# Performance work log

Hardware: AMD Instinct MI355X
Metric: run time of the kernel (lower is better)

## Reference

```python
import jax, jax.numpy as jnp
import numpy as np

N = 100000   # nodes
E = 300000   # edges
D = 256      # emb_dim
FD = 512     # feat_dim
L = 5        # num_layer
G = 4000     # num graphs
NUM_ATOM = 100
NUM_BOND = 2
EPS = 1e-5


def setup_inputs() -> dict:
    key = jax.random.key(0)
    ks = jax.random.split(key, 24)
    s = 0.02
    inp = {
        "atomics": jax.random.randint(ks[0], (N,), 0, NUM_ATOM, dtype=jnp.int32),
        "pos": jax.random.normal(ks[1], (N, 3), dtype=jnp.float32),
        "edge_index": jax.random.randint(ks[2], (2, E), 0, N, dtype=jnp.int32),
        "edge_attr": jax.random.randint(ks[3], (E,), 0, NUM_BOND, dtype=jnp.int32),
        "batch": jnp.sort(jax.random.randint(ks[4], (N,), 0, G, dtype=jnp.int32)),
        # parameters
        "x_emb1": jax.random.normal(ks[5], (NUM_ATOM, D)) * s,
        "x_emb2_w": jax.random.normal(ks[6], (3, D)) * s,
        "x_emb2_b": jnp.zeros((D,), jnp.float32),
        "edge_emb": jax.random.normal(ks[7], (L, NUM_BOND, D)) * s,
        "mlp_w1": jax.random.normal(ks[8], (L, D, 2 * D)) * s,
        "mlp_b1": jnp.zeros((L, 2 * D), jnp.float32),
        "mlp_w2": jax.random.normal(ks[9], (L, 2 * D, D)) * s,
        "mlp_b2": jnp.zeros((L, D), jnp.float32),
        "bn_gamma": jnp.ones((L, D), jnp.float32),
        "bn_beta": jnp.zeros((L, D), jnp.float32),
        "feat_w": jax.random.normal(ks[10], (D, FD)) * s,
        "feat_b": jnp.zeros((FD,), jnp.float32),
        "head_w1": jax.random.normal(ks[11], (FD, FD // 2)) * s,
        "head_b1": jnp.zeros((FD // 2,), jnp.float32),
        "head_w2": jax.random.normal(ks[12], (FD // 2, 1)) * s,
        "head_b2": jnp.zeros((1,), jnp.float32),
    }
    return inp


def reference(atomics, pos, edge_index, edge_attr, batch,
              x_emb1, x_emb2_w, x_emb2_b, edge_emb,
              mlp_w1, mlp_b1, mlp_w2, mlp_b2, bn_gamma, bn_beta,
              feat_w, feat_b, head_w1, head_b1, head_w2, head_b2):
    n = atomics.shape[0]
    # initial node features: atom-type embedding + linear(pos)
    h = x_emb1[atomics] + pos @ x_emb2_w + x_emb2_b
    # add self loops (self-loop bond type = NUM_BOND-1)
    loop = jnp.arange(n, dtype=edge_index.dtype)
    src = jnp.concatenate([edge_index[0], loop])           # x_j (source)
    dst = jnp.concatenate([edge_index[1], loop])           # aggregate target
    eattr = jnp.concatenate([edge_attr,
                             jnp.full((n,), NUM_BOND - 1, dtype=edge_attr.dtype)])
    for l in range(L):
        msg = h[src] + edge_emb[l][eattr]                  # [E+N, D]
        agg = jax.ops.segment_sum(msg, dst, num_segments=n)
        # GINEConv MLP: Linear -> Softplus -> Linear
        h = jax.nn.softplus(agg @ mlp_w1[l] + mlp_b1[l]) @ mlp_w2[l] + mlp_b2[l]
        # BatchNorm1d (training mode: batch statistics, biased var)
        mean = h.mean(axis=0)
        var = h.var(axis=0)
        h = (h - mean) / jnp.sqrt(var + EPS) * bn_gamma[l] + bn_beta[l]
        if l < L - 1:
            h = jax.nn.softplus(h)
        # dropout with drop_ratio=0 is a no-op
    feat = h @ feat_w + feat_b                             # [N, FD]
    # global mean pool over graphs
    ssum = jax.ops.segment_sum(feat, batch, num_segments=G)
    cnt = jax.ops.segment_sum(jnp.ones((n,), feat.dtype), batch, num_segments=G)
    gfeat = ssum / jnp.maximum(cnt, 1.0)[:, None]          # [G, FD]
    hid = jax.nn.softplus(gfeat @ head_w1 + head_b1)
    return hid @ head_w2 + head_b2                          # [G, 1]
```

## Files before the change

kernel.cpp:

```cpp
#include <hip/hip_runtime.h>
#include <hip/hip_bf16.h>
#include <hip/hip_fp16.h>
#include <stdint.h>

#define D_  256
#define FD_ 512
#define L_  5
#define EPS_ 1e-5f

#define PLANE_SH 1056
#define TILE_SH  4224

typedef unsigned short ushort_t;
typedef __attribute__((ext_vector_type(8))) _Float16 h8v;
typedef __attribute__((ext_vector_type(4))) float    f4v;

__device__ __forceinline__ float sp(float x) {
    float t = __expf(-fabsf(x));
    return fmaxf(x, 0.f) + __logf(1.f + t);
}

__device__ __forceinline__ ushort_t f2h_bits(float v) {
    union { _Float16 h; ushort_t u; } c;
    c.h = (_Float16)v;
    return c.u;
}

__device__ __forceinline__ float h2f(ushort_t u) {
    union { ushort_t u; _Float16 h; } c;
    c.u = u;
    return (float)c.h;
}

__device__ __forceinline__ size_t pk_off(int gm, int gn, int nKB) {
    return ((size_t)(gm >> 7) * nKB + (gn >> 5)) * TILE_SH
         + (size_t)((gn >> 3) & 3) * PLANE_SH
         + (gm & 127) * 8 + (gn & 7);
}

__global__ __launch_bounds__(256)
void init_h_kernel(const int* __restrict__ atomics, const float* __restrict__ pos,
                   const float* __restrict__ emb1, const float* __restrict__ w2,
                   const float* __restrict__ b2, ushort_t* __restrict__ h16, int N)
{
    int i = blockIdx.x;
    int d = threadIdx.x;
    int a = atomics[i];
    float p0 = pos[(size_t)i * 3 + 0];
    float p1 = pos[(size_t)i * 3 + 1];
    float p2 = pos[(size_t)i * 3 + 2];
    float v = emb1[(size_t)a * D_ + d]
            + p0 * w2[0 * D_ + d]
            + p1 * w2[1 * D_ + d]
            + p2 * w2[2 * D_ + d]
            + b2[d];
    h16[(size_t)i * D_ + d] = f2h_bits(v);
}

__global__ __launch_bounds__(256)
void hist_kernel(const int* __restrict__ dst, int* __restrict__ cnt, int E)
{
    int e = blockIdx.x * 256 + threadIdx.x;
    if (e < E) atomicAdd(&cnt[dst[e]], 1);
}

__global__ __launch_bounds__(256)
void alloc_kernel(const int* __restrict__ cnt, int* __restrict__ start,
                  int* __restrict__ cursor, int* __restrict__ total, int N)
{
    int i = blockIdx.x * 256 + threadIdx.x;
    if (i < N) {
        int s = atomicAdd(total, cnt[i]);
        start[i] = s;
        cursor[i] = s;
    }
}

__global__ __launch_bounds__(256)
void fill_kernel(const int* __restrict__ src, const int* __restrict__ dst,
                 const int* __restrict__ attr, int* __restrict__ cursor,
                 uint32_t* __restrict__ elist, int E)
{
    int e = blockIdx.x * 256 + threadIdx.x;
    if (e < E) {
        int p = atomicAdd(&cursor[dst[e]], 1);
        elist[p] = (uint32_t)src[e] | ((uint32_t)attr[e] << 30);
    }
}

__global__ __launch_bounds__(256)
void range_kernel(const int* __restrict__ batch, int* __restrict__ gstart,
                  int* __restrict__ gend, int N)
{
    int i = blockIdx.x * 256 + threadIdx.x;
    if (i >= N) return;
    int b = batch[i];
    if (i == 0 || batch[i - 1] != b) gstart[b] = i;
    if (i == N - 1 || batch[i + 1] != b) gend[b] = i + 1;
}

__global__ __launch_bounds__(256)
void act16_kernel(const ushort_t* __restrict__ h16, ushort_t* __restrict__ hact,
                  const float* __restrict__ bnsum, const float* __restrict__ gamma,
                  const float* __restrict__ beta, long long total8, float invN)
{
    __shared__ float ssc[256], ssh[256];
    int t = threadIdx.x;
    {
        float mean = bnsum[t] * invN;
        float var = bnsum[D_ + t] * invN - mean * mean;
        float sc = gamma[t] * rsqrtf(fmaxf(var, 0.f) + EPS_);
        ssc[t] = sc;
        ssh[t] = beta[t] - mean * sc;
    }
    __syncthreads();
    long long idx = (long long)blockIdx.x * 256 + t;
    if (idx >= total8) return;
    int c0 = (int)((idx * 8) & 255);
    uint4 in = *(const uint4*)(h16 + idx * 8);
    ushort_t* ip = (ushort_t*)&in;
    ushort_t ov[8];
#pragma unroll
    for (int j = 0; j < 8; ++j)
        ov[j] = f2h_bits(sp(h2f(ip[j]) * ssc[c0 + j] + ssh[c0 + j]));
    *(uint4*)(hact + idx * 8) = *(uint4*)ov;
}

__global__ __launch_bounds__(256)
void gather_pack4_kernel(const ushort_t* __restrict__ hact, const uint32_t* __restrict__ elist,
                         const int* __restrict__ start, const int* __restrict__ cnt,
                         const float* __restrict__ ee_l, ushort_t* __restrict__ aggP, int N)
{
    int i0 = blockIdx.x * 4;
    int d = threadIdx.x;
    float ee0 = ee_l[d];
    float ee1 = ee_l[D_ + d];
    float acc[4];
#pragma unroll
    for (int r = 0; r < 4; ++r) {
        int i = i0 + r;
        if (i >= N) { acc[r] = 0.f; continue; }
        float a = h2f(hact[(size_t)i * D_ + d]) + ee1;
        int base = start[i], deg = cnt[i];
        for (int j = 0; j < deg; ++j) {
            uint32_t p = elist[base + j];
            int s = p & 0x3FFFFFFF;
            a += h2f(hact[(size_t)s * D_ + d]) + ((p >> 30) ? ee1 : ee0);
        }
        acc[r] = a;
    }
#pragma unroll
    for (int r = 0; r < 4; ++r) {
        int i = i0 + r;
        if (i < N) aggP[pk_off(i, d, 8)] = f2h_bits(acc[r]);
    }
}

__global__ __launch_bounds__(256)
void pool_bn_kernel(const ushort_t* __restrict__ h16, const float* __restrict__ bnsum,
                    const float* __restrict__ gamma, const float* __restrict__ beta,
                    const int* __restrict__ gstart, const int* __restrict__ gend,
                    ushort_t* __restrict__ poolP, float invN)
{
    int g = blockIdx.x;
    int d = threadIdx.x;
    float mean = bnsum[d] * invN;
    float var = bnsum[D_ + d] * invN - mean * mean;
    float sc = gamma[d] * rsqrtf(fmaxf(var, 0.f) + EPS_);
    float sh = beta[d] - mean * sc;
    int s0 = gstart[g], s1 = gend[g];
    float acc = 0.f;
    int i = s0;
    for (; i + 4 <= s1; i += 4) {
        float a0 = h2f(h16[(size_t)(i + 0) * D_ + d]);
        float a1 = h2f(h16[(size_t)(i + 1) * D_ + d]);
        float a2 = h2f(h16[(size_t)(i + 2) * D_ + d]);
        float a3 = h2f(h16[(size_t)(i + 3) * D_ + d]);
        acc += (a0 + a1) + (a2 + a3);
    }
    for (; i < s1; ++i)
        acc += h2f(h16[(size_t)i * D_ + d]);
    int cnt = s1 - s0;
    float mval = (cnt > 0) ? (sc * acc / (float)cnt + sh) : 0.f;
    poolP[pk_off(g, d, 8)] = f2h_bits(mval);
}

__global__ __launch_bounds__(256)
void convert_w_pack(const float* __restrict__ W, ushort_t* __restrict__ dh,
                    int N, int nKB)
{
    int kb = blockIdx.x, nb = blockIdx.y;
    int n = threadIdx.x >> 1, half = threadIdx.x & 1;
#pragma unroll
    for (int j = 0; j < 2; ++j) {
        int kq = half * 2 + j;
        size_t o = (size_t)(nb * nKB + kb) * TILE_SH + kq * PLANE_SH + n * 8;
#pragma unroll
        for (int jj = 0; jj < 8; ++jj) {
            float w = W[(size_t)(kb * 32 + kq * 8 + jj) * N + nb * 128 + n];
            dh[o + jj] = f2h_bits(w);
        }
    }
}

__global__ __launch_bounds__(512, 4)
void fused_mlp_kernel(const ushort_t* __restrict__ APK,
                      const ushort_t* __restrict__ W1P,
                      const ushort_t* __restrict__ W2P,
                      const float* __restrict__ b1,
                      const float* __restrict__ b2,
                      ushort_t* __restrict__ Hout,
                      float* __restrict__ bnsum,
                      int m)
{
    __shared__ ushort_t Tl[32768];

    int rb = blockIdx.x;
    int tid = threadIdx.x, w = tid >> 6, lane = tid & 63;
    int fr = lane & 15, kq = lane >> 4;

    const ushort_t* aT = APK + (size_t)(rb >> 1) * (8 * TILE_SH)
                       + (size_t)kq * PLANE_SH + (size_t)((rb & 1) * 64 + fr) * 8;
    const ushort_t* bT = W1P + (size_t)(w >> 1) * (8 * TILE_SH)
                       + (size_t)kq * PLANE_SH + (size_t)((w & 1) * 64 + fr) * 8;

    f4v acc1[4][4];
#pragma unroll
    for (int i = 0; i < 4; ++i)
#pragma unroll
        for (int j = 0; j < 4; ++j)
            acc1[i][j] = (f4v){0.f, 0.f, 0.f, 0.f};

    for (int kb = 0; kb < 8; ++kb) {
        h8v Af[4], Bf[4];
#pragma unroll
        for (int t = 0; t < 4; ++t) {
            Af[t] = *(const h8v*)(aT + (size_t)kb * TILE_SH + t * 128);
            Bf[t] = *(const h8v*)(bT + (size_t)kb * TILE_SH + t * 128);
        }
        __builtin_amdgcn_s_setprio(1);
#pragma unroll
        for (int rt = 0; rt < 4; ++rt)
#pragma unroll
            for (int ct = 0; ct < 4; ++ct)
                acc1[rt][ct] = __builtin_amdgcn_mfma_f32_16x16x32_f16(
                    Af[rt], Bf[ct], acc1[rt][ct], 0, 0, 0);
        __builtin_amdgcn_s_setprio(0);
    }

#pragma unroll
    for (int ct = 0; ct < 4; ++ct) {
        float bv = b1[w * 64 + ct * 16 + fr];
        int base = (w * 2 + (ct >> 1)) * 2048
                 + ((( fr >> 3) + ct * 2) & 3) * 512
                 + (fr & 7);
#pragma unroll
        for (int rt = 0; rt < 4; ++rt)
#pragma unroll
            for (int rr = 0; rr < 4; ++rr) {
                int row = rt * 16 + kq * 4 + rr;
                Tl[base + row * 8] = f2h_bits(sp(acc1[rt][ct][rr] + bv));
            }
    }
    __syncthreads();

    const ushort_t* wT = W2P + (size_t)(w >> 2) * (16 * TILE_SH)
                       + (size_t)kq * PLANE_SH + (size_t)((w & 3) * 32 + fr) * 8;

    f4v acc2[4][2];
#pragma unroll
    for (int i = 0; i < 4; ++i)
#pragma unroll
        for (int j = 0; j < 2; ++j)
            acc2[i][j] = (f4v){0.f, 0.f, 0.f, 0.f};

    for (int kb = 0; kb < 16; ++kb) {
        h8v Tf[4], Wf[2];
#pragma unroll
        for (int t = 0; t < 4; ++t)
            Tf[t] = *(const h8v*)(Tl + kb * 2048 + kq * 512 + (fr + t * 16) * 8);
#pragma unroll
        for (int t = 0; t < 2; ++t)
            Wf[t] = *(const h8v*)(wT + (size_t)kb * TILE_SH + t * 128);
        __builtin_amdgcn_s_setprio(1);
#pragma unroll
        for (int rt = 0; rt < 4; ++rt)
#pragma unroll
            for (int ct = 0; ct < 2; ++ct)
                acc2[rt][ct] = __builtin_amdgcn_mfma_f32_16x16x32_f16(
                    Tf[rt], Wf[ct], acc2[rt][ct], 0, 0, 0);
        __builtin_amdgcn_s_setprio(0);
    }

    int gm0 = rb * 64 + kq * 4;
#pragma unroll
    for (int ct = 0; ct < 2; ++ct) {
        int gn = w * 32 + ct * 16 + fr;
        float bv = b2[gn];
        float s = 0.f, ss = 0.f;
#pragma unroll
        for (int rt = 0; rt < 4; ++rt)
#pragma unroll
            for (int rr = 0; rr < 4; ++rr) {
                int gm = gm0 + rt * 16 + rr;
                if (gm < m) {
                    float v = acc2[rt][ct][rr] + bv;
                    Hout[(size_t)gm * D_ + gn] = f2h_bits(v);
                    s += v;
                    ss += v * v;
                }
            }
        s  += __shfl_xor(s, 16);  s  += __shfl_xor(s, 32);
        ss += __shfl_xor(ss, 16); ss += __shfl_xor(ss, 32);
        if (kq == 0) {
            atomicAdd(&bnsum[gn], s);
            atomicAdd(&bnsum[D_ + gn], ss);
        }
    }
}

template <int EPI>
__global__ __launch_bounds__(256, 3)
void gemm_p16(const ushort_t* __restrict__ APK, const ushort_t* __restrict__ BPK,
              const float* __restrict__ bias,
              ushort_t* __restrict__ Tout, float* __restrict__ Cout,
              float* __restrict__ bnsum, const int* __restrict__ batch,
              int m, int N, int nKB)
{
    const int NB = N >> 7;
    const int mb = (m + 127) >> 7;
    int id = blockIdx.x;
    int grp = id / (8 * NB);
    int rem = id - grp * 8 * NB;
    int nb = rem >> 3;
    int rb = grp * 8 + (rem & 7);
    if (rb >= mb) return;

    int tid = threadIdx.x, wave = tid >> 6, lane = tid & 63;
    int wr = wave >> 1, wc = wave & 1;
    int fr = lane & 15, kq = lane >> 4;

    const ushort_t* aP = APK + (size_t)rb * nKB * TILE_SH
                       + (size_t)kq * PLANE_SH + (size_t)(wr * 64 + fr) * 8;
    const ushort_t* bP = BPK + (size_t)nb * nKB * TILE_SH
                       + (size_t)kq * PLANE_SH + (size_t)(wc * 64 + fr) * 8;

    f4v acc[4][4];
#pragma unroll
    for (int i = 0; i < 4; ++i)
#pragma unroll
        for (int j = 0; j < 4; ++j)
            acc[i][j] = (f4v){0.f, 0.f, 0.f, 0.f};

    h8v Fa[4], Fb[4], Ga[4], Gb[4];

#define LOADF(dA, dB, kbi)                                                   \
    {   const ushort_t* ap_ = aP + (size_t)(kbi) * TILE_SH;                  \
        const ushort_t* bp_ = bP + (size_t)(kbi) * TILE_SH;                  \
        _Pragma("unroll")                                                    \
        for (int t = 0; t < 4; ++t) {                                        \
            dA[t] = *(const h8v*)(ap_ + t * 128);                            \
            dB[t] = *(const h8v*)(bp_ + t * 128);                            \
        } }

#define MFMA16(sA, sB)                                                       \
    {   __builtin_amdgcn_s_setprio(1);                                       \
        _Pragma("unroll")                                                    \
        for (int rt = 0; rt < 4; ++rt)                                       \
            _Pragma("unroll")                                                \
            for (int ct = 0; ct < 4; ++ct)                                   \
                acc[rt][ct] = __builtin_amdgcn_mfma_f32_16x16x32_f16(        \
                    sA[rt], sB[ct], acc[rt][ct], 0, 0, 0);                   \
        __builtin_amdgcn_s_setprio(0); }

    LOADF(Fa, Fb, 0);
    for (int kb = 0; kb < nKB; kb += 2) {
        LOADF(Ga, Gb, kb + 1);
        MFMA16(Fa, Fb);
        if (kb + 2 < nKB) LOADF(Fa, Fb, kb + 2);
        MFMA16(Ga, Gb);
    }
#undef LOADF
#undef MFMA16

    int gm00 = rb * 128 + wr * 64 + kq * 4;
    int gn0  = nb * 128 + wc * 64 + fr;
    int nKBo = N >> 5;
    size_t tileRow = (size_t)(rb * nKBo + nb * 4 + wc * 2) * TILE_SH
                   + (size_t)((wr * 64 + kq * 4) * 8 + (fr & 7));
#pragma unroll
    for (int ct = 0; ct < 4; ++ct) {
        int gn = gn0 + ct * 16;
        float bv = bias[gn];
        float s = 0.f, ss = 0.f;
        size_t cb = tileRow + (size_t)(ct >> 1) * TILE_SH
                  + (size_t)((2 * ct + (fr >> 3)) & 3) * PLANE_SH;
#pragma unroll
        for (int rt = 0; rt < 4; ++rt) {
            if (EPI == 2) {
                int bp = -1; float run = 0.f;
#pragma unroll
                for (int rr = 0; rr < 4; ++rr) {
                    int gm = gm00 + rt * 16 + rr;
                    if (gm >= m) continue;
                    float v = acc[rt][ct][rr] + bv;
                    int bg = batch[gm];
                    if (bg == bp) { run += v; }
                    else {
                        if (bp >= 0) atomicAdd(&Cout[(size_t)bp * N + gn], run);
                        bp = bg; run = v;
                    }
                }
                if (bp >= 0) atomicAdd(&Cout[(size_t)bp * N + gn], run);
            } else {
#pragma unroll
                for (int rr = 0; rr < 4; ++rr) {
                    int gm = gm00 + rt * 16 + rr;
                    if (gm >= m) continue;
                    float v = acc[rt][ct][rr] + bv;
                    if (EPI == 0) {
                        Tout[cb + (rt * 16 + rr) * 8] = f2h_bits(sp(v));
                    } else if (EPI == 1) {
                        Tout[(size_t)gm * N + gn] = f2h_bits(v);
                        s += v;
                        ss += v * v;
                    } else {
                        Cout[(size_t)gm * N + gn] = v;
                    }
                }
            }
        }
        if (EPI == 1) {
            s  += __shfl_xor(s, 16);  s  += __shfl_xor(s, 32);
            ss += __shfl_xor(ss, 16); ss += __shfl_xor(ss, 32);
            if (kq == 0) {
                atomicAdd(&bnsum[gn], s);
                atomicAdd(&bnsum[D_ + gn], ss);
            }
        }
    }
}

#define BM 64
#define BN 64
#define BK 16

__global__ __launch_bounds__(256)
void gemm_head(const float* __restrict__ A, const float* __restrict__ W,
               const float* __restrict__ bias, float* __restrict__ C,
               int M, int N, int K)
{
    __shared__ float As[BK][BM + 4];
    __shared__ float Ws[BK][BN + 4];

    int tid = threadIdx.x;
    int bm = blockIdx.y * BM;
    int bn = blockIdx.x * BN;
    int tx = tid & 15;
    int ty = tid >> 4;

    float acc[4][4] = {};

    int a_m = tid >> 2;
    int a_k = (tid & 3) * 4;
    int w_k = tid >> 4;
    int w_n = (tid & 15) * 4;

    for (int k0 = 0; k0 < K; k0 += BK) {
        int gm = bm + a_m;
        float4 av = make_float4(0.f, 0.f, 0.f, 0.f);
        if (gm < M)
            av = *(const float4*)(A + (size_t)gm * K + k0 + a_k);
        As[a_k + 0][a_m] = av.x;
        As[a_k + 1][a_m] = av.y;
        As[a_k + 2][a_m] = av.z;
        As[a_k + 3][a_m] = av.w;

        float4 wv = *(const float4*)(W + (size_t)(k0 + w_k) * N + bn + w_n);
        *(float4*)&Ws[w_k][w_n] = wv;

        __syncthreads();

#pragma unroll
        for (int k = 0; k < BK; ++k) {
            float4 a4 = *(const float4*)&As[k][ty * 4];
            float4 b4 = *(const float4*)&Ws[k][tx * 4];
            float a[4] = {a4.x, a4.y, a4.z, a4.w};
            float b[4] = {b4.x, b4.y, b4.z, b4.w};
#pragma unroll
            for (int i = 0; i < 4; ++i)
#pragma unroll
                for (int j = 0; j < 4; ++j)
                    acc[i][j] += a[i] * b[j];
        }
        __syncthreads();
    }

#pragma unroll
    for (int i = 0; i < 4; ++i) {
        int gm = bm + ty * 4 + i;
        if (gm >= M) continue;
#pragma unroll
        for (int j = 0; j < 4; ++j) {
            int gn = bn + tx * 4 + j;
            C[(size_t)gm * N + gn] = sp(acc[i][j] + bias[gn]);
        }
    }
}

__global__ __launch_bounds__(256)
void head2_kernel(const float* __restrict__ hid, const float* __restrict__ w2,
                  const float* __restrict__ b2, float* __restrict__ out, int G)
{
    __shared__ float red[256];
    int g = blockIdx.x;
    int t = threadIdx.x;
    float v = hid[(size_t)g * 256 + t] * w2[t];
    red[t] = v;
    __syncthreads();
    for (int s = 128; s > 0; s >>= 1) {
        if (t < s) red[t] += red[t + s];
        __syncthreads();
    }
    if (t == 0) out[g] = red[0] + b2[0];
}

extern "C" void kernel_launch(void* const* d_in, const int* in_sizes, int n_in,
                              void* d_out, int out_size, void* d_ws, size_t ws_size,
                              hipStream_t stream)
{
    const int N = in_sizes[0];
    const int E = in_sizes[3];
    const int G = out_size;

    const int*   atomics  = (const int*)d_in[0];
    const float* pos      = (const float*)d_in[1];
    const int*   eidx     = (const int*)d_in[2];
    const int*   eattr    = (const int*)d_in[3];
    const int*   batch    = (const int*)d_in[4];
    const float* x_emb1   = (const float*)d_in[5];
    const float* x_emb2_w = (const float*)d_in[6];
    const float* x_emb2_b = (const float*)d_in[7];
    const float* edge_emb = (const float*)d_in[8];
    const float* mlp_w1   = (const float*)d_in[9];
    const float* mlp_b1   = (const float*)d_in[10];
    const float* mlp_w2   = (const float*)d_in[11];
    const float* mlp_b2   = (const float*)d_in[12];
    const float* bn_g     = (const float*)d_in[13];
    const float* bn_b     = (const float*)d_in[14];
    const float* feat_w   = (const float*)d_in[15];
    const float* feat_b   = (const float*)d_in[16];
    const float* head_w1  = (const float*)d_in[17];
    const float* head_b1  = (const float*)d_in[18];
    const float* head_w2  = (const float*)d_in[19];
    const float* head_b2  = (const float*)d_in[20];
    float* out = (float*)d_out;

    const int* src = eidx;
    const int* dst = eidx + E;

    char* ws = (char*)d_ws;
    size_t off = 0;
    auto carve = [&](size_t bytes) {
        void* p = ws + off;
        off += (bytes + 255) & ~(size_t)255;
        return p;
    };

    const int nRB = (N + 127) / 128;
    const int nGB = (G + 127) / 128;

    ushort_t* h16  = (ushort_t*)carve((size_t)N * D_ * 2);
    ushort_t* hact = (ushort_t*)carve((size_t)N * D_ * 2);
    ushort_t* aggP = (ushort_t*)carve((size_t)nRB * 8 * TILE_SH * 2);
    const size_t WTILES = 32 * TILE_SH;
    ushort_t* w1P = (ushort_t*)carve((size_t)L_ * WTILES * 2);
    ushort_t* w2P = (ushort_t*)carve((size_t)L_ * WTILES * 2);
    ushort_t* fP  = (ushort_t*)carve(WTILES * 2);
    float* bnsum  = (float*)carve(2 * D_ * 4);
    float* gfeat  = (float*)carve((size_t)G * FD_ * 4);
    float* hid    = (float*)carve((size_t)G * (FD_ / 2) * 4);
    ushort_t* poolP = (ushort_t*)carve((size_t)nGB * 8 * TILE_SH * 2);
    int* gstart  = (int*)carve((size_t)G * 4);
    int* gend    = (int*)carve((size_t)G * 4);
    int* cnt_i   = (int*)carve((size_t)N * 4);
    int* start_i = (int*)carve((size_t)N * 4);
    int* cursor  = (int*)carve((size_t)N * 4);
    int* total   = (int*)carve(4);
    uint32_t* elist = (uint32_t*)carve((size_t)E * 4);

    const float invN = 1.f / (float)N;

    hipMemsetAsync(cnt_i, 0, (size_t)N * 4, stream);
    hipMemsetAsync(total, 0, 4, stream);
    hipMemsetAsync(gstart, 0, (size_t)G * 4, stream);
    hipMemsetAsync(gend, 0, (size_t)G * 4, stream);
    hist_kernel<<<(E + 255) / 256, 256, 0, stream>>>(dst, cnt_i, E);
    alloc_kernel<<<(N + 255) / 256, 256, 0, stream>>>(cnt_i, start_i, cursor, total, N);
    fill_kernel<<<(E + 255) / 256, 256, 0, stream>>>(src, dst, eattr, cursor, elist, E);
    range_kernel<<<(N + 255) / 256, 256, 0, stream>>>(batch, gstart, gend, N);

    for (int l = 0; l < L_; ++l) {
        convert_w_pack<<<dim3(8, 4), 256, 0, stream>>>(
            mlp_w1 + (size_t)l * D_ * FD_, w1P + (size_t)l * WTILES, FD_, 8);
        convert_w_pack<<<dim3(16, 2), 256, 0, stream>>>(
            mlp_w2 + (size_t)l * FD_ * D_, w2P + (size_t)l * WTILES, D_, 16);
    }
    convert_w_pack<<<dim3(8, 4), 256, 0, stream>>>(feat_w, fP, FD_, 8);

    init_h_kernel<<<N, 256, 0, stream>>>(atomics, pos, x_emb1, x_emb2_w, x_emb2_b, h16, N);

    const long long total8 = (long long)N * D_ / 8;
    const int ACTB = (int)((total8 + 255) / 256);
    const int GB4 = (N + 3) / 4;
    const int FB  = (N + 63) / 64;

    for (int l = 0; l < L_; ++l) {
        const float* ee_l = edge_emb + (size_t)l * 2 * D_;
        const ushort_t* gsrc = h16;
        if (l > 0) {
            act16_kernel<<<ACTB, 256, 0, stream>>>(h16, hact, bnsum,
                bn_g + (size_t)(l - 1) * D_, bn_b + (size_t)(l - 1) * D_, total8, invN);
            gsrc = hact;
        }
        gather_pack4_kernel<<<GB4, 256, 0, stream>>>(gsrc, elist, start_i, cnt_i,
                                                     ee_l, aggP, N);

        hipMemsetAsync(bnsum, 0, 2 * D_ * 4, stream);
        fused_mlp_kernel<<<FB, 512, 0, stream>>>(
            aggP, w1P + (size_t)l * WTILES, w2P + (size_t)l * WTILES,
            mlp_b1 + (size_t)l * FD_, mlp_b2 + (size_t)l * D_,
            h16, bnsum, N);
    }

    pool_bn_kernel<<<G, 256, 0, stream>>>(h16, bnsum, bn_g + (size_t)(L_ - 1) * D_,
                                          bn_b + (size_t)(L_ - 1) * D_,
                                          gstart, gend, poolP, invN);
    auto swgrid = [](int mb, int NBc) { return ((mb + 7) / 8) * 8 * NBc; };
    gemm_p16<3><<<swgrid(nGB, 4), 256, 0, stream>>>(
        poolP, fP, feat_b, nullptr, gfeat, nullptr, nullptr, G, FD_, 8);

    gemm_head<<<dim3((FD_ / 2) / BN, (G + BM - 1) / BM), 256, 0, stream>>>(
        gfeat, head_w1, head_b1, hid, G, FD_ / 2, FD_);
    head2_kernel<<<G, 256, 0, stream>>>(hid, head_w2, head_b2, out, G);
}
```

Measured before the change: 1.273 ms.

## Fuse BN+softplus activation into gather, batch 8 nodes, swap MFMA operand order

Drops the separate activation kernel and applies the batch-norm affine plus softplus inside the gather, on every neighbour load. This removes a full read and write of the node features per layer. The cost is recomputing softplus once per edge (about 4x per node) instead of once per node. The gather now handles 8 nodes per block and issues their edge loads interleaved so more memory requests are in flight, at the price of divergent loops padded to the block's maximum degree. The first MLP GEMM swaps its MFMA operands, which lets the softplus output be written to shared memory as packed 4-element stores with vectorised bias loads instead of scalar stores.

```diff
diff --git a/kernel.cpp b/kernel.cpp
--- a/kernel.cpp
+++ b/kernel.cpp
@@ -30,6 +30,10 @@
     union { ushort_t u; _Float16 h; } c;
     c.u = u;
     return (float)c.h;
+}
+
+__device__ __forceinline__ uint32_t pk2(float a, float b) {
+    return (uint32_t)f2h_bits(a) | ((uint32_t)f2h_bits(b) << 16);
 }
 
 __device__ __forceinline__ size_t pk_off(int gm, int gn, int nKB) {
@@ -99,60 +103,65 @@
     if (i == N - 1 || batch[i + 1] != b) gend[b] = i + 1;
 }
 
-__global__ __launch_bounds__(256)
-void act16_kernel(const ushort_t* __restrict__ h16, ushort_t* __restrict__ hact,
-                  const float* __restrict__ bnsum, const float* __restrict__ gamma,
-                  const float* __restrict__ beta, long long total8, float invN)
-{
-    __shared__ float ssc[256], ssh[256];
-    int t = threadIdx.x;
-    {
-        float mean = bnsum[t] * invN;
-        float var = bnsum[D_ + t] * invN - mean * mean;
-        float sc = gamma[t] * rsqrtf(fmaxf(var, 0.f) + EPS_);
-        ssc[t] = sc;
-        ssh[t] = beta[t] - mean * sc;
-    }
-    __syncthreads();
-    long long idx = (long long)blockIdx.x * 256 + t;
-    if (idx >= total8) return;
-    int c0 = (int)((idx * 8) & 255);
-    uint4 in = *(const uint4*)(h16 + idx * 8);
-    ushort_t* ip = (ushort_t*)&in;
-    ushort_t ov[8];
-#pragma unroll
-    for (int j = 0; j < 8; ++j)
-        ov[j] = f2h_bits(sp(h2f(ip[j]) * ssc[c0 + j] + ssh[c0 + j]));
-    *(uint4*)(hact + idx * 8) = *(uint4*)ov;
-}
-
-__global__ __launch_bounds__(256)
-void gather_pack4_kernel(const ushort_t* __restrict__ hact, const uint32_t* __restrict__ elist,
-                         const int* __restrict__ start, const int* __restrict__ cnt,
-                         const float* __restrict__ ee_l, ushort_t* __restrict__ aggP, int N)
-{
-    int i0 = blockIdx.x * 4;
+template <int DOACT>
+__global__ __launch_bounds__(256)
+void gather_act8_kernel(const ushort_t* __restrict__ h16, const uint32_t* __restrict__ elist,
+                        const int* __restrict__ start, const int* __restrict__ cnt,
+                        const float* __restrict__ ee_l,
+                        const float* __restrict__ bnsum, const float* __restrict__ gamma,
+                        const float* __restrict__ beta, float invN,
+                        ushort_t* __restrict__ aggP, int N)
+{
+    int i0 = blockIdx.x * 8;
     int d = threadIdx.x;
+    float sc = 1.f, sh = 0.f;
+    if (DOACT) {
+        float mean = bnsum[d] * invN;
+        float var = bnsum[D_ + d] * invN - mean * mean;
+        sc = gamma[d] * rsqrtf(fmaxf(var, 0.f) + EPS_);
+        sh = beta[d] - mean * sc;
+    }
     float ee0 = ee_l[d];
     float ee1 = ee_l[D_ + d];
-    float acc[4];
-#pragma unroll
-    for (int r = 0; r < 4; ++r) {
+    int base[8], deg[8];
+    float a[8];
+    int mdeg = 0;
+#pragma unroll
+    for (int r = 0; r < 8; ++r) {
         int i = i0 + r;
-        if (i >= N) { acc[r] = 0.f; continue; }
-        float a = h2f(hact[(size_t)i * D_ + d]) + ee1;
-        int base = start[i], deg = cnt[i];
-        for (int j = 0; j < deg; ++j) {
-            uint32_t p = elist[base + j];
-            int s = p & 0x3FFFFFFF;
-            a += h2f(hact[(size_t)s * D_ + d]) + ((p >> 30) ? ee1 : ee0);
-        }
-        acc[r] = a;
-    }
-#pragma unroll
-    for (int r = 0; r < 4; ++r) {
+        base[r] = 0; deg[r] = 0; a[r] = 0.f;
+        if (i < N) {
+            base[r] = start[i];
+            deg[r] = cnt[i];
+            float v = h2f(h16[(size_t)i * D_ + d]);
+            if (DOACT) v = sp(v * sc + sh);
+            a[r] = v + ee1;
+            mdeg = (deg[r] > mdeg) ? deg[r] : mdeg;
+        }
+    }
+    for (int j = 0; j < mdeg; ++j) {
+        uint32_t p[8];
+#pragma unroll
+        for (int r = 0; r < 8; ++r) {
+            int idx = (j < deg[r]) ? (base[r] + j) : 0;
+            p[r] = elist[idx];
+        }
+        float v[8];
+#pragma unroll
+        for (int r = 0; r < 8; ++r) {
+            int s = p[r] & 0x3FFFFFFF;
+            float t = h2f(h16[(size_t)s * D_ + d]);
+            if (DOACT) t = sp(t * sc + sh);
+            v[r] = t + ((p[r] >> 30) ? ee1 : ee0);
+        }
+#pragma unroll
+        for (int r = 0; r < 8; ++r)
+            if (j < deg[r]) a[r] += v[r];
+    }
+#pragma unroll
+    for (int r = 0; r < 8; ++r) {
         int i = i0 + r;
-        if (i < N) aggP[pk_off(i, d, 8)] = f2h_bits(acc[r]);
+        if (i < N) aggP[pk_off(i, d, 8)] = f2h_bits(a[r]);
     }
 }
 
@@ -232,35 +241,35 @@
             acc1[i][j] = (f4v){0.f, 0.f, 0.f, 0.f};
 
     for (int kb = 0; kb < 8; ++kb) {
-        h8v Af[4], Bf[4];
+        h8v Af[4], Wf[4];
 #pragma unroll
         for (int t = 0; t < 4; ++t) {
             Af[t] = *(const h8v*)(aT + (size_t)kb * TILE_SH + t * 128);
-            Bf[t] = *(const h8v*)(bT + (size_t)kb * TILE_SH + t * 128);
+            Wf[t] = *(const h8v*)(bT + (size_t)kb * TILE_SH + t * 128);
         }
         __builtin_amdgcn_s_setprio(1);
 #pragma unroll
-        for (int rt = 0; rt < 4; ++rt)
-#pragma unroll
-            for (int ct = 0; ct < 4; ++ct)
-                acc1[rt][ct] = __builtin_amdgcn_mfma_f32_16x16x32_f16(
-                    Af[rt], Bf[ct], acc1[rt][ct], 0, 0, 0);
+        for (int nt = 0; nt < 4; ++nt)
+#pragma unroll
+            for (int mt = 0; mt < 4; ++mt)
+                acc1[nt][mt] = __builtin_amdgcn_mfma_f32_16x16x32_f16(
+                    Wf[nt], Af[mt], acc1[nt][mt], 0, 0, 0);
         __builtin_amdgcn_s_setprio(0);
     }
 
 #pragma unroll
-    for (int ct = 0; ct < 4; ++ct) {
-        float bv = b1[w * 64 + ct * 16 + fr];
-        int base = (w * 2 + (ct >> 1)) * 2048
-                 + ((( fr >> 3) + ct * 2) & 3) * 512
-                 + (fr & 7);
-#pragma unroll
-        for (int rt = 0; rt < 4; ++rt)
-#pragma unroll
-            for (int rr = 0; rr < 4; ++rr) {
-                int row = rt * 16 + kq * 4 + rr;
-                Tl[base + row * 8] = f2h_bits(sp(acc1[rt][ct][rr] + bv));
-            }
+    for (int nt = 0; nt < 4; ++nt) {
+        float4 b1v = *(const float4*)(b1 + w * 64 + nt * 16 + kq * 4);
+        int baseu = (w * 2 + (nt >> 1)) * 2048
+                  + ((nt & 1) * 2 + (kq >> 1)) * 512
+                  + (kq & 1) * 4;
+#pragma unroll
+        for (int mt = 0; mt < 4; ++mt) {
+            uint2 val;
+            val.x = pk2(sp(acc1[nt][mt][0] + b1v.x), sp(acc1[nt][mt][1] + b1v.y));
+            val.y = pk2(sp(acc1[nt][mt][2] + b1v.z), sp(acc1[nt][mt][3] + b1v.w));
+            *(uint2*)(Tl + baseu + (mt * 16 + fr) * 8) = val;
+        }
     }
     __syncthreads();
 
@@ -571,7 +580,6 @@
     const int nGB = (G + 127) / 128;
 
     ushort_t* h16  = (ushort_t*)carve((size_t)N * D_ * 2);
-    ushort_t* hact = (ushort_t*)carve((size_t)N * D_ * 2);
     ushort_t* aggP = (ushort_t*)carve((size_t)nRB * 8 * TILE_SH * 2);
     const size_t WTILES = 32 * TILE_SH;
     ushort_t* w1P = (ushort_t*)carve((size_t)L_ * WTILES * 2);
@@ -610,21 +618,21 @@
 
     init_h_kernel<<<N, 256, 0, stream>>>(atomics, pos, x_emb1, x_emb2_w, x_emb2_b, h16, N);
 
-    const long long total8 = (long long)N * D_ / 8;
-    const int ACTB = (int)((total8 + 255) / 256);
-    const int GB4 = (N + 3) / 4;
+    const int GB8 = (N + 7) / 8;
     const int FB  = (N + 63) / 64;
 
     for (int l = 0; l < L_; ++l) {
         const float* ee_l = edge_emb + (size_t)l * 2 * D_;
-        const ushort_t* gsrc = h16;
-        if (l > 0) {
-            act16_kernel<<<ACTB, 256, 0, stream>>>(h16, hact, bnsum,
-                bn_g + (size_t)(l - 1) * D_, bn_b + (size_t)(l - 1) * D_, total8, invN);
-            gsrc = hact;
-        }
-        gather_pack4_kernel<<<GB4, 256, 0, stream>>>(gsrc, elist, start_i, cnt_i,
-                                                     ee_l, aggP, N);
+        if (l == 0) {
+            gather_act8_kernel<0><<<GB8, 256, 0, stream>>>(
+                h16, elist, start_i, cnt_i, ee_l,
+                bnsum, bn_g, bn_b, invN, aggP, N);
+        } else {
+            gather_act8_kernel<1><<<GB8, 256, 0, stream>>>(
+                h16, elist, start_i, cnt_i, ee_l,
+                bnsum, bn_g + (size_t)(l - 1) * D_, bn_b + (size_t)(l - 1) * D_,
+                invN, aggP, N);
+        }
 
         hipMemsetAsync(bnsum, 0, 2 * D_ * 4, stream);
         fused_mlp_kernel<<<FB, 512, 0, stream>>>(
```

Result: slower. 1.310 ms (+2.9%).
